# Performance work log

Hardware: AMD Instinct MI355X
Metric: run time of the kernel (lower is better)

## Reference

```python
import jax, jax.numpy as jnp
import numpy as np

KERNEL_SIZE = 5  # k, local correlation window
EPS = 1e-6


def local_self_correlation(x, k):
    """x: (b,c,h,w) -> (b,k^2,h,w). For each of the k^2 shifts (dy,dx) compute
    sum_c x[..., y+dy, x+dx] * x[..., y, x] with zero padding at borders."""
    pad = k // 2
    b, c, h, w = x.shape
    xp = jnp.pad(x, ((0, 0), (0, 0), (pad, pad), (pad, pad)))
    outs = []
    for dy in range(-pad, pad + 1):  # fixed small loop over k^2 shifts
        for dx in range(-pad, pad + 1):
            nb = xp[:, :, pad + dy:pad + dy + h, pad + dx:pad + dx + w]
            outs.append(jnp.sum(nb * x, axis=1))  # (b,h,w)
    return jnp.stack(outs, axis=1)  # (b,k^2,h,w)


def feature_l2norm(f):
    norm = jnp.sqrt(jnp.sum(f * f, axis=1, keepdims=True) + EPS)
    return f / norm


def setup_inputs() -> dict:
    key = jax.random.key(0)
    k1, k2, k3 = jax.random.split(key, 3)
    b, c, h, w = 8, 1024, 64, 64
    hidden = 1024
    in_dim = c + KERNEL_SIZE * KERNEL_SIZE  # 1049
    x = jax.random.normal(k1, (b, c, h, w), dtype=jnp.float32)
    W = jax.random.normal(k2, (hidden, in_dim), dtype=jnp.float32) * 0.02
    bias = jax.random.normal(k3, (hidden,), dtype=jnp.float32) * 0.02
    return {"x": x, "W": W, "b": bias}


def reference(x, W, b):
    feature_gs = local_self_correlation(x, KERNEL_SIZE)      # (b,k^2,h,w)
    feature_gs = feature_l2norm(feature_gs)
    feature_cat = jnp.concatenate([x, feature_gs], axis=1)    # (b,c+k^2,h,w)
    # 1x1 conv == channel GEMM, then ReLU
    out = jnp.einsum('bihw,oi->bohw', feature_cat, W) + b[None, :, None, None]
    return jax.nn.relu(out)
```

## Files before the change

### kernel.cpp

```cpp
#include <hip/hip_runtime.h>

typedef __attribute__((ext_vector_type(8))) short bf16x8;
typedef __attribute__((ext_vector_type(4))) float f32x4;

__device__ __forceinline__ unsigned short f2bf(float f) {
    unsigned int u = __float_as_uint(f);
    unsigned int r = (u + 0x7fffu + ((u >> 16) & 1u)) >> 16;
    return (unsigned short)r;
}

#define KPAD 1088
#define NT   17

__global__ void kWb_conv(const float* __restrict__ W, unsigned short* __restrict__ Wb)
{
    const int o = blockIdx.x;
    for (int k = threadIdx.x; k < KPAD; k += 256) {
        float v = (k < 1049) ? W[(size_t)o * 1049 + k] : 0.f;
        Wb[(size_t)o * KPAD + k] = f2bf(v);
    }
}

__global__ __launch_bounds__(256) void kT_conv(const float* __restrict__ x,
                                               unsigned short* __restrict__ xT)
{
    __shared__ unsigned short tile[64][128];
    const int bid = blockIdx.x;
    const int mst = bid >> 3;
    const int ct  = bid & 7;
    const int m0  = mst * 64;
    const int b   = m0 >> 12, ms0 = m0 & 4095;
    const int t   = threadIdx.x;
    const int msq = (t & 15) * 4;
    const int cg  = t >> 4;
    const int c0  = ct * 128 + cg * 8;

    const float* src = x + ((size_t)b * 1024 + c0) * 4096 + ms0 + msq;
    float4 v[8];
    #pragma unroll
    for (int j = 0; j < 8; ++j)
        v[j] = *(const float4*)(src + (size_t)j * 4096);

    #pragma unroll
    for (int p = 0; p < 4; ++p) {
        unsigned int w[4];
        #pragma unroll
        for (int q = 0; q < 4; ++q) {
            float lo = ((const float*)&v[2 * q])[p];
            float hi = ((const float*)&v[2 * q + 1])[p];
            w[q] = (unsigned int)f2bf(lo) | ((unsigned int)f2bf(hi) << 16);
        }
        const int row = msq + p;
        const int pch = cg ^ ((row >> 2) & 15);
        *(uint4*)&tile[row][pch * 8] = make_uint4(w[0], w[1], w[2], w[3]);
    }
    __syncthreads();

    #pragma unroll
    for (int q = 0; q < 4; ++q) {
        const int flat = q * 256 + t;
        const int row  = flat >> 4, ch = flat & 15;
        const int pch  = ch ^ ((row >> 2) & 15);
        uint4 val = *(const uint4*)&tile[row][pch * 8];
        *(uint4*)((char*)xT + (size_t)(m0 + row) * (KPAD * 2) + (size_t)(ct * 128 + ch * 8) * 2) = val;
    }
}

__global__ __launch_bounds__(256, 2) void k1a_corr(const float* __restrict__ x,
                                                   float* __restrict__ fpart)
{
    __shared__ float slab[2][20][68];
    const int bid   = blockIdx.x;
    const int split = bid & 15;
    const int b     = (bid >> 4) & 7;
    const int rg    = bid >> 7;
    const int y0    = rg * 16;
    const int t     = threadIdx.x;
    const int tc    = t & 15, tr = t >> 4;
    const int cs    = tc * 4;

    if (t < 160) {
        int buf = t / 80, rem = t % 80;
        int r = rem >> 2, cc = rem & 3;
        slab[buf][r][(cc < 2) ? cc : (64 + cc)] = 0.f;
    }

    float acc[25][4];
    #pragma unroll
    for (int s = 0; s < 25; ++s)
        #pragma unroll
        for (int p = 0; p < 4; ++p) acc[s][p] = 0.f;

    const float* xb = x + ((size_t)b * 1024 + split * 64) * 4096;

    const int r0 = t >> 4,         c40 = t & 15;
    const int y0r0 = y0 - 2 + r0;
    const int r1 = (t + 256) >> 4, c41 = t & 15;
    const int y0r1 = y0 - 2 + r1;
    const bool has1 = (t < 64);

    #define K1A_LOAD(ch, VA, VB)                                                \
        {                                                                        \
            const float* s_ = xb + (size_t)(ch) * 4096;                          \
            VA = (y0r0 >= 0 && y0r0 < 64) ? *(const float4*)(s_ + y0r0 * 64 + c40 * 4) \
                                          : make_float4(0.f, 0.f, 0.f, 0.f);     \
            if (has1)                                                            \
                VB = (y0r1 >= 0 && y0r1 < 64) ? *(const float4*)(s_ + y0r1 * 64 + c41 * 4) \
                                              : make_float4(0.f, 0.f, 0.f, 0.f); \
        }
    #define K1A_WRITE(buf, VA, VB)                                               \
        {                                                                        \
            float2* d0 = (float2*)&slab[buf][r0][2 + c40 * 4];                   \
            d0[0] = make_float2(VA.x, VA.y);                                     \
            d0[1] = make_float2(VA.z, VA.w);                                     \
            if (has1) {                                                          \
                float2* d1 = (float2*)&slab[buf][r1][2 + c41 * 4];               \
                d1[0] = make_float2(VB.x, VB.y);                                 \
                d1[1] = make_float2(VB.z, VB.w);                                 \
            }                                                                    \
        }
    #define K1A_COMPUTE(buf)                                                     \
        {                                                                        \
            const float* base = &slab[buf][tr][cs];                              \
            float ctr[4], wf[8];                                                 \
            {                                                                    \
                const float4* pr = (const float4*)(base + 2 * 68);               \
                float4 a = pr[0], b4 = pr[1];                                    \
                wf[0]=a.x; wf[1]=a.y; wf[2]=a.z; wf[3]=a.w;                      \
                wf[4]=b4.x; wf[5]=b4.y; wf[6]=b4.z; wf[7]=b4.w;                  \
                ctr[0]=wf[2]; ctr[1]=wf[3]; ctr[2]=wf[4]; ctr[3]=wf[5];          \
                _Pragma("unroll")                                                \
                for (int dx = -2; dx <= 2; ++dx)                                 \
                    _Pragma("unroll")                                            \
                    for (int p = 0; p < 4; ++p)                                  \
                        acc[10 + dx + 2][p] += wf[p + 2 + dx] * ctr[p];          \
            }                                                                    \
            _Pragma("unroll")                                                    \
            for (int r = 0; r < 5; ++r) {                                        \
                if (r == 2) continue;                                            \
                const float4* pr = (const float4*)(base + r * 68);               \
                float4 a = pr[0], b4 = pr[1];                                    \
                wf[0]=a.x; wf[1]=a.y; wf[2]=a.z; wf[3]=a.w;                      \
                wf[4]=b4.x; wf[5]=b4.y; wf[6]=b4.z; wf[7]=b4.w;                  \
                _Pragma("unroll")                                                \
                for (int dx = -2; dx <= 2; ++dx)                                 \
                    _Pragma("unroll")                                            \
                    for (int p = 0; p < 4; ++p)                                  \
                        acc[r * 5 + dx + 2][p] += wf[p + 2 + dx] * ctr[p];       \
            }                                                                    \
        }

    float4 Sa0, Sa1, Sb0, Sb1;
    K1A_LOAD(0, Sa0, Sa1)
    K1A_LOAD(1, Sb0, Sb1)
    K1A_WRITE(0, Sa0, Sa1)
    K1A_LOAD(2, Sa0, Sa1)
    __syncthreads();

    for (int i = 0; i < 64; i += 2) {
        K1A_WRITE(1, Sb0, Sb1)
        K1A_LOAD(min(i + 3, 63), Sb0, Sb1)
        K1A_COMPUTE(0)
        __syncthreads();
        K1A_WRITE(0, Sa0, Sa1)
        K1A_LOAD(min(i + 4, 63), Sa0, Sa1)
        K1A_COMPUTE(1)
        __syncthreads();
    }
    #undef K1A_LOAD
    #undef K1A_WRITE
    #undef K1A_COMPUTE

    const int mbase = b * 4096 + (y0 + tr) * 64 + cs;
    #pragma unroll
    for (int s = 0; s < 25; ++s) {
        *(float4*)(fpart + (size_t)(split * 25 + s) * 32768 + mbase) =
            make_float4(acc[s][0], acc[s][1], acc[s][2], acc[s][3]);
    }
}

__global__ void k1b_norm(const float* __restrict__ fpart, unsigned short* __restrict__ xT)
{
    const int m = blockIdx.x * 256 + threadIdx.x;
    float f[25];
    #pragma unroll
    for (int s = 0; s < 25; ++s) {
        float v = 0.f;
        #pragma unroll
        for (int sp = 0; sp < 16; ++sp)
            v += fpart[(size_t)(sp * 25 + s) * 32768 + m];
        f[s] = v;
    }
    float ss = 1e-6f;
    #pragma unroll
    for (int s = 0; s < 25; ++s) ss += f[s] * f[s];
    const float inv = 1.f / sqrtf(ss);

    unsigned int w[16];
    #pragma unroll
    for (int q = 0; q < 16; ++q) w[q] = 0u;
    #pragma unroll
    for (int s = 0; s < 25; ++s) {
        unsigned int h = f2bf(f[s] * inv);
        w[s >> 1] |= h << ((s & 1) * 16);
    }
    uint4* dst = (uint4*)((char*)xT + (size_t)m * (KPAD * 2) + 2048);
    dst[0] = make_uint4(w[0],  w[1],  w[2],  w[3]);
    dst[1] = make_uint4(w[4],  w[5],  w[6],  w[7]);
    dst[2] = make_uint4(w[8],  w[9],  w[10], w[11]);
    dst[3] = make_uint4(w[12], w[13], w[14], w[15]);
    uint4 z = make_uint4(0u, 0u, 0u, 0u);
    dst[4] = z; dst[5] = z; dst[6] = z; dst[7] = z;
}

__global__ __launch_bounds__(512, 2) void kgemm(const unsigned short* __restrict__ xT,
                                                const unsigned short* __restrict__ Wb,
                                                const float* __restrict__ bias,
                                                float* __restrict__ out)
{
    __shared__ unsigned short LA[2][256][64];
    __shared__ unsigned short LB[2][256][64];

    const int bid = blockIdx.x;
    const int wg  = (bid & 7) * 64 + (bid >> 3);
    const int mt  = wg >> 2, nt = wg & 3;
    const int m0  = mt * 256, n0 = nt * 256;
    const int t   = threadIdx.x;
    const int l   = t & 63, w = t >> 6;
    const int lr  = l & 15, kq = l >> 4;
    const int wm  = w >> 2, wn = w & 3;

    const int sr = l >> 3;
    const int sp = (l & 7) ^ sr;
    const unsigned short* gA = xT + (size_t)(m0 + w * 8 + sr) * KPAD + sp * 8;
    const unsigned short* gB = Wb + (size_t)(n0 + w * 8 + sr) * KPAD + sp * 8;

    auto STAGE = [&](int tt, int half) {
        if ((unsigned)tt >= NT) return;
        const int db = tt & 1;
        const size_t ko = (size_t)tt * 64;
        if (half < 2) {
            const unsigned short* g = gA + (size_t)(half * 128) * KPAD + ko;
            __builtin_amdgcn_global_load_lds((const void*)g,
                (void*)&LA[db][half * 128 + w * 8][0], 16, 0, 0);
            __builtin_amdgcn_global_load_lds((const void*)(g + (size_t)64 * KPAD),
                (void*)&LA[db][half * 128 + 64 + w * 8][0], 16, 0, 0);
        } else {
            const int hb = half - 2;
            const unsigned short* g = gB + (size_t)(hb * 128) * KPAD + ko;
            __builtin_amdgcn_global_load_lds((const void*)g,
                (void*)&LB[db][hb * 128 + w * 8][0], 16, 0, 0);
            __builtin_amdgcn_global_load_lds((const void*)(g + (size_t)64 * KPAD),
                (void*)&LB[db][hb * 128 + 64 + w * 8][0], 16, 0, 0);
        }
    };

    f32x4 zero = {0.f, 0.f, 0.f, 0.f};
    f32x4 acc[8][4];
    #pragma unroll
    for (int i = 0; i < 8; ++i)
        #pragma unroll
        for (int j = 0; j < 4; ++j) acc[i][j] = zero;

    bf16x8 a0[4][2], a1[4][2], b0[2][2], b1[2][2];

    #define LDA(dst, DB, ih)                                                     \
        _Pragma("unroll")                                                        \
        for (int i = 0; i < 4; ++i) {                                            \
            _Pragma("unroll")                                                    \
            for (int ks = 0; ks < 2; ++ks) {                                     \
                const int row = wm * 128 + ((ih) * 4 + i) * 16 + lr;             \
                const int slot = (ks * 4 + kq) ^ (row & 7);                      \
                dst[i][ks] = *(const bf16x8*)&LA[DB][row][slot * 8];             \
            }                                                                    \
        }
    #define LDB(dst, DB, jh)                                                     \
        _Pragma("unroll")                                                        \
        for (int j = 0; j < 2; ++j) {                                            \
            _Pragma("unroll")                                                    \
            for (int ks = 0; ks < 2; ++ks) {                                     \
                const int row = wn * 64 + ((jh) * 2 + j) * 16 + lr;              \
                const int slot = (ks * 4 + kq) ^ (row & 7);                      \
                dst[j][ks] = *(const bf16x8*)&LB[DB][row][slot * 8];             \
            }                                                                    \
        }
    #define MM(A, B, i0, j0)                                                     \
        _Pragma("unroll")                                                        \
        for (int ks = 0; ks < 2; ++ks) {                                         \
            _Pragma("unroll")                                                    \
            for (int i = 0; i < 4; ++i) {                                        \
                _Pragma("unroll")                                                \
                for (int j = 0; j < 2; ++j)                                      \
                    acc[(i0) + i][(j0) + j] = __builtin_amdgcn_mfma_f32_16x16x32_bf16( \
                        A[i][ks], B[j][ks], acc[(i0) + i][(j0) + j], 0, 0, 0);   \
            }                                                                    \
        }

    #define TILE(DB, TT)                                                         \
    {                                                                            \
        const int tti = (TT);                                                    \
                      \
        LDA(a0, DB, 0)                                                           \
        LDB(b0, DB, 0)                                                           \
        STAGE(tti + 1, 1);                                                       \
        asm volatile("s_waitcnt lgkmcnt(8)" ::: "memory");                       \
        __builtin_amdgcn_s_barrier();                                            \
        asm volatile("s_waitcnt lgkmcnt(0)" ::: "memory");                       \
        __builtin_amdgcn_sched_barrier(0);                                       \
        __builtin_amdgcn_s_setprio(1);                                           \
        MM(a0, b0, 0, 0)                                                         \
        __builtin_amdgcn_s_setprio(0);                                           \
        __builtin_amdgcn_s_barrier();                                            \
                      \
        LDA(a1, DB, 1)                                                           \
        LDB(b1, DB, 1)                                                           \
        STAGE(tti + 1, 3);                                                       \
        asm volatile("s_waitcnt lgkmcnt(8)" ::: "memory");                       \
        __builtin_amdgcn_s_barrier();                                            \
        asm volatile("s_waitcnt lgkmcnt(0)" ::: "memory");                       \
        __builtin_amdgcn_sched_barrier(0);                                       \
        __builtin_amdgcn_s_setprio(1);                                           \
        MM(a0, b1, 0, 2)                                                         \
        __builtin_amdgcn_s_setprio(0);                                           \
        __builtin_amdgcn_s_barrier();                                            \
            \
        STAGE(tti + 2, 0);                                                       \
        __builtin_amdgcn_s_barrier();                                            \
        __builtin_amdgcn_s_setprio(1);                                           \
        MM(a1, b0, 4, 0)                                                         \
        __builtin_amdgcn_s_setprio(0);                                           \
        __builtin_amdgcn_s_barrier();                                            \
             \
        STAGE(tti + 2, 2);                                                       \
        __builtin_amdgcn_s_barrier();                                            \
        __builtin_amdgcn_s_setprio(1);                                           \
        MM(a1, b1, 4, 2)                                                         \
        __builtin_amdgcn_s_setprio(0);                                           \
        if (tti + 2 < NT) {                                                      \
            asm volatile("s_waitcnt vmcnt(4)" ::: "memory");                     \
        } else {                                                                 \
            asm volatile("s_waitcnt vmcnt(0)" ::: "memory");                     \
        }                                                                        \
        __builtin_amdgcn_s_barrier();                                            \
    }

    STAGE(0, 0); STAGE(0, 2); STAGE(0, 1); STAGE(0, 3);
    STAGE(1, 0); STAGE(1, 2);
    asm volatile("s_waitcnt vmcnt(4)" ::: "memory");
    __builtin_amdgcn_s_barrier();

    int tt = 0;
    #pragma unroll 1
    for (int it = 0; it < (NT - 1) / 2; ++it, tt += 2) {
        TILE(0, tt)
        TILE(1, tt + 1)
    }
    TILE(0, NT - 1)

    const int bb = m0 >> 12;
    const int ms = (m0 & 4095) + wm * 128 + kq * 4;
    #pragma unroll
    for (int j = 0; j < 4; ++j) {
        const int n = n0 + wn * 64 + j * 16 + lr;
        const float bv = bias[n];
        float* ob = out + (size_t)bb * 4194304 + (size_t)n * 4096 + ms;
        #pragma unroll
        for (int i = 0; i < 8; ++i) {
            f32x4 v = acc[i][j];
            float4 o = make_float4(fmaxf(v[0] + bv, 0.f), fmaxf(v[1] + bv, 0.f),
                                   fmaxf(v[2] + bv, 0.f), fmaxf(v[3] + bv, 0.f));
            *(float4*)(ob + i * 16) = o;
        }
    }
    #undef LDA
    #undef LDB
    #undef MM
    #undef TILE
}

extern "C" void kernel_launch(void* const* d_in, const int* in_sizes, int n_in,
                              void* d_out, int out_size, void* d_ws, size_t ws_size,
                              hipStream_t stream)
{
    const float* x    = (const float*)d_in[0];
    const float* W    = (const float*)d_in[1];
    const float* bias = (const float*)d_in[2];
    float* out        = (float*)d_out;

    char* ws = (char*)d_ws;
    unsigned short* xT = (unsigned short*)ws;
    unsigned short* Wb = (unsigned short*)(ws + 71303168);
    float* fpart       = (float*)d_out;

    kWb_conv<<<1024, 256, 0, stream>>>(W, Wb);
    kT_conv <<<4096, 256, 0, stream>>>(x, xT);
    k1a_corr<<<512,  256, 0, stream>>>(x, fpart);
    k1b_norm<<<128,  256, 0, stream>>>(fpart, xT);
    kgemm   <<<512,  512, 0, stream>>>(xT, Wb, bias, out);
}
```

Before: 203.5 us.

## Merge front-end kernels into one launch and reorder GEMM tile MFMA phases

Merges the W bf16 conversion, the x transpose/convert, and the local correlation into a single kernel that branches on block index. The goal is to cut launch overhead and let the compute-heavy correlation blocks overlap with the memory-bound conversion blocks. Separately, the GEMM tile loop now runs its MFMA quadrants in a different order, and the A-fragment LDS load moves later, which shortens how long those registers stay live. The shared launch bounds of (256, 2) now apply to the conversion blocks too, and the combined kernel carries the correlation path's register pressure, which may lower occupancy for those blocks.

```diff
diff --git a/kernel.cpp b/kernel.cpp
--- a/kernel.cpp
+++ b/kernel.cpp
@@ -12,170 +12,170 @@
 #define KPAD 1088
 #define NT   17
 
-__global__ void kWb_conv(const float* __restrict__ W, unsigned short* __restrict__ Wb)
+__global__ __launch_bounds__(256, 2) void kfront(const float* __restrict__ x,
+                                                 const float* __restrict__ W,
+                                                 unsigned short* __restrict__ xT,
+                                                 unsigned short* __restrict__ Wb,
+                                                 float* __restrict__ fpart)
 {
-    const int o = blockIdx.x;
-    for (int k = threadIdx.x; k < KPAD; k += 256) {
-        float v = (k < 1049) ? W[(size_t)o * 1049 + k] : 0.f;
-        Wb[(size_t)o * KPAD + k] = f2bf(v);
-    }
-}
-
-__global__ __launch_bounds__(256) void kT_conv(const float* __restrict__ x,
-                                               unsigned short* __restrict__ xT)
-{
-    __shared__ unsigned short tile[64][128];
-    const int bid = blockIdx.x;
-    const int mst = bid >> 3;
-    const int ct  = bid & 7;
-    const int m0  = mst * 64;
-    const int b   = m0 >> 12, ms0 = m0 & 4095;
-    const int t   = threadIdx.x;
-    const int msq = (t & 15) * 4;
-    const int cg  = t >> 4;
-    const int c0  = ct * 128 + cg * 8;
-
-    const float* src = x + ((size_t)b * 1024 + c0) * 4096 + ms0 + msq;
-    float4 v[8];
-    #pragma unroll
-    for (int j = 0; j < 8; ++j)
-        v[j] = *(const float4*)(src + (size_t)j * 4096);
-
-    #pragma unroll
-    for (int p = 0; p < 4; ++p) {
-        unsigned int w[4];
+    __shared__ float4 lds_raw[1024];
+    const int gbid = blockIdx.x;
+    const int t    = threadIdx.x;
+
+    if (gbid < 512) {
+        float (*slab)[20][68] = (float (*)[20][68])lds_raw;
+        const int bid   = gbid;
+        const int split = bid & 15;
+        const int b     = (bid >> 4) & 7;
+        const int rg    = bid >> 7;
+        const int y0    = rg * 16;
+        const int tc    = t & 15, tr = t >> 4;
+        const int cs    = tc * 4;
+
+        if (t < 160) {
+            int buf = t / 80, rem = t % 80;
+            int r = rem >> 2, cc = rem & 3;
+            slab[buf][r][(cc < 2) ? cc : (64 + cc)] = 0.f;
+        }
+
+        float acc[25][4];
+        #pragma unroll
+        for (int s = 0; s < 25; ++s)
+            #pragma unroll
+            for (int p = 0; p < 4; ++p) acc[s][p] = 0.f;
+
+        const float* xb = x + ((size_t)b * 1024 + split * 64) * 4096;
+
+        const int r0 = t >> 4,         c40 = t & 15;
+        const int y0r0 = y0 - 2 + r0;
+        const int r1 = (t + 256) >> 4, c41 = t & 15;
+        const int y0r1 = y0 - 2 + r1;
+        const bool has1 = (t < 64);
+
+        #define K1A_LOAD(ch, VA, VB)                                                \
+            {                                                                        \
+                const float* s_ = xb + (size_t)(ch) * 4096;                          \
+                VA = (y0r0 >= 0 && y0r0 < 64) ? *(const float4*)(s_ + y0r0 * 64 + c40 * 4) \
+                                              : make_float4(0.f, 0.f, 0.f, 0.f);     \
+                if (has1)                                                            \
+                    VB = (y0r1 >= 0 && y0r1 < 64) ? *(const float4*)(s_ + y0r1 * 64 + c41 * 4) \
+                                                  : make_float4(0.f, 0.f, 0.f, 0.f); \
+            }
+        #define K1A_WRITE(buf, VA, VB)                                               \
+            {                                                                        \
+                float2* d0 = (float2*)&slab[buf][r0][2 + c40 * 4];                   \
+                d0[0] = make_float2(VA.x, VA.y);                                     \
+                d0[1] = make_float2(VA.z, VA.w);                                     \
+                if (has1) {                                                          \
+                    float2* d1 = (float2*)&slab[buf][r1][2 + c41 * 4];               \
+                    d1[0] = make_float2(VB.x, VB.y);                                 \
+                    d1[1] = make_float2(VB.z, VB.w);                                 \
+                }                                                                    \
+            }
+        #define K1A_COMPUTE(buf)                                                     \
+            {                                                                        \
+                const float* base = &slab[buf][tr][cs];                              \
+                float ctr[4], wf[8];                                                 \
+                {                                                                    \
+                    const float4* pr = (const float4*)(base + 2 * 68);               \
+                    float4 a = pr[0], b4 = pr[1];                                    \
+                    wf[0]=a.x; wf[1]=a.y; wf[2]=a.z; wf[3]=a.w;                      \
+                    wf[4]=b4.x; wf[5]=b4.y; wf[6]=b4.z; wf[7]=b4.w;                  \
+                    ctr[0]=wf[2]; ctr[1]=wf[3]; ctr[2]=wf[4]; ctr[3]=wf[5];          \
+                    _Pragma("unroll")                                                \
+                    for (int dx = -2; dx <= 2; ++dx)                                 \
+                        _Pragma("unroll")                                            \
+                        for (int p = 0; p < 4; ++p)                                  \
+                            acc[10 + dx + 2][p] += wf[p + 2 + dx] * ctr[p];          \
+                }                                                                    \
+                _Pragma("unroll")                                                    \
+                for (int r = 0; r < 5; ++r) {                                        \
+                    if (r == 2) continue;                                            \
+                    const float4* pr = (const float4*)(base + r * 68);               \
+                    float4 a = pr[0], b4 = pr[1];                                    \
+                    wf[0]=a.x; wf[1]=a.y; wf[2]=a.z; wf[3]=a.w;                      \
+                    wf[4]=b4.x; wf[5]=b4.y; wf[6]=b4.z; wf[7]=b4.w;                  \
+                    _Pragma("unroll")                                                \
+                    for (int dx = -2; dx <= 2; ++dx)                                 \
+                        _Pragma("unroll")                                            \
+                        for (int p = 0; p < 4; ++p)                                  \
+                            acc[r * 5 + dx + 2][p] += wf[p + 2 + dx] * ctr[p];       \
+                }                                                                    \
+            }
+
+        float4 Sa0, Sa1, Sb0, Sb1;
+        K1A_LOAD(0, Sa0, Sa1)
+        K1A_LOAD(1, Sb0, Sb1)
+        K1A_WRITE(0, Sa0, Sa1)
+        K1A_LOAD(2, Sa0, Sa1)
+        __syncthreads();
+
+        for (int i = 0; i < 64; i += 2) {
+            K1A_WRITE(1, Sb0, Sb1)
+            K1A_LOAD(min(i + 3, 63), Sb0, Sb1)
+            K1A_COMPUTE(0)
+            __syncthreads();
+            K1A_WRITE(0, Sa0, Sa1)
+            K1A_LOAD(min(i + 4, 63), Sa0, Sa1)
+            K1A_COMPUTE(1)
+            __syncthreads();
+        }
+        #undef K1A_LOAD
+        #undef K1A_WRITE
+        #undef K1A_COMPUTE
+
+        const int mbase = b * 4096 + (y0 + tr) * 64 + cs;
+        #pragma unroll
+        for (int s = 0; s < 25; ++s) {
+            *(float4*)(fpart + (size_t)(split * 25 + s) * 32768 + mbase) =
+                make_float4(acc[s][0], acc[s][1], acc[s][2], acc[s][3]);
+        }
+    } else if (gbid < 4608) {
+        unsigned short (*tile)[128] = (unsigned short (*)[128])lds_raw;
+        const int bid = gbid - 512;
+        const int mst = bid >> 3;
+        const int ct  = bid & 7;
+        const int m0  = mst * 64;
+        const int b   = m0 >> 12, ms0 = m0 & 4095;
+        const int msq = (t & 15) * 4;
+        const int cg  = t >> 4;
+        const int c0  = ct * 128 + cg * 8;
+
+        const float* src = x + ((size_t)b * 1024 + c0) * 4096 + ms0 + msq;
+        float4 v[8];
+        #pragma unroll
+        for (int j = 0; j < 8; ++j)
+            v[j] = *(const float4*)(src + (size_t)j * 4096);
+
+        #pragma unroll
+        for (int p = 0; p < 4; ++p) {
+            unsigned int w[4];
+            #pragma unroll
+            for (int q = 0; q < 4; ++q) {
+                float lo = ((const float*)&v[2 * q])[p];
+                float hi = ((const float*)&v[2 * q + 1])[p];
+                w[q] = (unsigned int)f2bf(lo) | ((unsigned int)f2bf(hi) << 16);
+            }
+            const int row = msq + p;
+            const int pch = cg ^ ((row >> 2) & 15);
+            *(uint4*)&tile[row][pch * 8] = make_uint4(w[0], w[1], w[2], w[3]);
+        }
+        __syncthreads();
+
         #pragma unroll
         for (int q = 0; q < 4; ++q) {
-            float lo = ((const float*)&v[2 * q])[p];
-            float hi = ((const float*)&v[2 * q + 1])[p];
-            w[q] = (unsigned int)f2bf(lo) | ((unsigned int)f2bf(hi) << 16);
-        }
-        const int row = msq + p;
-        const int pch = cg ^ ((row >> 2) & 15);
-        *(uint4*)&tile[row][pch * 8] = make_uint4(w[0], w[1], w[2], w[3]);
-    }
-    __syncthreads();
-
-    #pragma unroll
-    for (int q = 0; q < 4; ++q) {
-        const int flat = q * 256 + t;
-        const int row  = flat >> 4, ch = flat & 15;
-        const int pch  = ch ^ ((row >> 2) & 15);
-        uint4 val = *(const uint4*)&tile[row][pch * 8];
-        *(uint4*)((char*)xT + (size_t)(m0 + row) * (KPAD * 2) + (size_t)(ct * 128 + ch * 8) * 2) = val;
-    }
-}
-
-__global__ __launch_bounds__(256, 2) void k1a_corr(const float* __restrict__ x,
-                                                   float* __restrict__ fpart)
-{
-    __shared__ float slab[2][20][68];
-    const int bid   = blockIdx.x;
-    const int split = bid & 15;
-    const int b     = (bid >> 4) & 7;
-    const int rg    = bid >> 7;
-    const int y0    = rg * 16;
-    const int t     = threadIdx.x;
-    const int tc    = t & 15, tr = t >> 4;
-    const int cs    = tc * 4;
-
-    if (t < 160) {
-        int buf = t / 80, rem = t % 80;
-        int r = rem >> 2, cc = rem & 3;
-        slab[buf][r][(cc < 2) ? cc : (64 + cc)] = 0.f;
-    }
-
-    float acc[25][4];
-    #pragma unroll
-    for (int s = 0; s < 25; ++s)
-        #pragma unroll
-        for (int p = 0; p < 4; ++p) acc[s][p] = 0.f;
-
-    const float* xb = x + ((size_t)b * 1024 + split * 64) * 4096;
-
-    const int r0 = t >> 4,         c40 = t & 15;
-    const int y0r0 = y0 - 2 + r0;
-    const int r1 = (t + 256) >> 4, c41 = t & 15;
-    const int y0r1 = y0 - 2 + r1;
-    const bool has1 = (t < 64);
-
-    #define K1A_LOAD(ch, VA, VB)                                                \
-        {                                                                        \
-            const float* s_ = xb + (size_t)(ch) * 4096;                          \
-            VA = (y0r0 >= 0 && y0r0 < 64) ? *(const float4*)(s_ + y0r0 * 64 + c40 * 4) \
-                                          : make_float4(0.f, 0.f, 0.f, 0.f);     \
-            if (has1)                                                            \
-                VB = (y0r1 >= 0 && y0r1 < 64) ? *(const float4*)(s_ + y0r1 * 64 + c41 * 4) \
-                                              : make_float4(0.f, 0.f, 0.f, 0.f); \
-        }
-    #define K1A_WRITE(buf, VA, VB)                                               \
-        {                                                                        \
-            float2* d0 = (float2*)&slab[buf][r0][2 + c40 * 4];                   \
-            d0[0] = make_float2(VA.x, VA.y);                                     \
-            d0[1] = make_float2(VA.z, VA.w);                                     \
-            if (has1) {                                                          \
-                float2* d1 = (float2*)&slab[buf][r1][2 + c41 * 4];               \
-                d1[0] = make_float2(VB.x, VB.y);                                 \
-                d1[1] = make_float2(VB.z, VB.w);                                 \
-            }                                                                    \
-        }
-    #define K1A_COMPUTE(buf)                                                     \
-        {                                                                        \
-            const float* base = &slab[buf][tr][cs];                              \
-            float ctr[4], wf[8];                                                 \
-            {                                                                    \
-                const float4* pr = (const float4*)(base + 2 * 68);               \
-                float4 a = pr[0], b4 = pr[1];                                    \
-                wf[0]=a.x; wf[1]=a.y; wf[2]=a.z; wf[3]=a.w;                      \
-                wf[4]=b4.x; wf[5]=b4.y; wf[6]=b4.z; wf[7]=b4.w;                  \
-                ctr[0]=wf[2]; ctr[1]=wf[3]; ctr[2]=wf[4]; ctr[3]=wf[5];          \
-                _Pragma("unroll")                                                \
-                for (int dx = -2; dx <= 2; ++dx)                                 \
-                    _Pragma("unroll")                                            \
-                    for (int p = 0; p < 4; ++p)                                  \
-                        acc[10 + dx + 2][p] += wf[p + 2 + dx] * ctr[p];          \
-            }                                                                    \
-            _Pragma("unroll")                                                    \
-            for (int r = 0; r < 5; ++r) {                                        \
-                if (r == 2) continue;                                            \
-                const float4* pr = (const float4*)(base + r * 68);               \
-                float4 a = pr[0], b4 = pr[1];                                    \
-                wf[0]=a.x; wf[1]=a.y; wf[2]=a.z; wf[3]=a.w;                      \
-                wf[4]=b4.x; wf[5]=b4.y; wf[6]=b4.z; wf[7]=b4.w;                  \
-                _Pragma("unroll")                                                \
-                for (int dx = -2; dx <= 2; ++dx)                                 \
-                    _Pragma("unroll")                                            \
-                    for (int p = 0; p < 4; ++p)                                  \
-                        acc[r * 5 + dx + 2][p] += wf[p + 2 + dx] * ctr[p];       \
-            }                                                                    \
-        }
-
-    float4 Sa0, Sa1, Sb0, Sb1;
-    K1A_LOAD(0, Sa0, Sa1)
-    K1A_LOAD(1, Sb0, Sb1)
-    K1A_WRITE(0, Sa0, Sa1)
-    K1A_LOAD(2, Sa0, Sa1)
-    __syncthreads();
-
-    for (int i = 0; i < 64; i += 2) {
-        K1A_WRITE(1, Sb0, Sb1)
-        K1A_LOAD(min(i + 3, 63), Sb0, Sb1)
-        K1A_COMPUTE(0)
-        __syncthreads();
-        K1A_WRITE(0, Sa0, Sa1)
-        K1A_LOAD(min(i + 4, 63), Sa0, Sa1)
-        K1A_COMPUTE(1)
-        __syncthreads();
-    }
-    #undef K1A_LOAD
-    #undef K1A_WRITE
-    #undef K1A_COMPUTE
-
-    const int mbase = b * 4096 + (y0 + tr) * 64 + cs;
-    #pragma unroll
-    for (int s = 0; s < 25; ++s) {
-        *(float4*)(fpart + (size_t)(split * 25 + s) * 32768 + mbase) =
-            make_float4(acc[s][0], acc[s][1], acc[s][2], acc[s][3]);
+            const int flat = q * 256 + t;
+            const int row  = flat >> 4, ch = flat & 15;
+            const int pch  = ch ^ ((row >> 2) & 15);
+            uint4 val = *(const uint4*)&tile[row][pch * 8];
+            *(uint4*)((char*)xT + (size_t)(m0 + row) * (KPAD * 2) + (size_t)(ct * 128 + ch * 8) * 2) = val;
+        }
+    } else {
+        const int o = gbid - 4608;
+        for (int k = t; k < KPAD; k += 256) {
+            float v = (k < 1049) ? W[(size_t)o * 1049 + k] : 0.f;
+            Wb[(size_t)o * KPAD + k] = f2bf(v);
+        }
     }
 }
 
@@ -299,7 +299,7 @@
     #define TILE(DB, TT)                                                         \
     {                                                                            \
         const int tti = (TT);                                                    \
-                      \
+                          \
         LDA(a0, DB, 0)                                                           \
         LDB(b0, DB, 0)                                                           \
         STAGE(tti + 1, 1);                                                       \
@@ -311,11 +311,9 @@
         MM(a0, b0, 0, 0)                                                         \
         __builtin_amdgcn_s_setprio(0);                                           \
         __builtin_amdgcn_s_barrier();                                            \
-                      \
-        LDA(a1, DB, 1)                                                           \
+                                \
         LDB(b1, DB, 1)                                                           \
         STAGE(tti + 1, 3);                                                       \
-        asm volatile("s_waitcnt lgkmcnt(8)" ::: "memory");                       \
         __builtin_amdgcn_s_barrier();                                            \
         asm volatile("s_waitcnt lgkmcnt(0)" ::: "memory");                       \
         __builtin_amdgcn_sched_barrier(0);                                       \
@@ -323,18 +321,21 @@
         MM(a0, b1, 0, 2)                                                         \
         __builtin_amdgcn_s_setprio(0);                                           \
         __builtin_amdgcn_s_barrier();                                            \
+           \
+        LDA(a1, DB, 1)                                                           \
+        STAGE(tti + 2, 0);                                                       \
+        __builtin_amdgcn_s_barrier();                                            \
+        asm volatile("s_waitcnt lgkmcnt(0)" ::: "memory");                       \
+        __builtin_amdgcn_sched_barrier(0);                                       \
+        __builtin_amdgcn_s_setprio(1);                                           \
+        MM(a1, b1, 4, 2)                                                         \
+        __builtin_amdgcn_s_setprio(0);                                           \
+        __builtin_amdgcn_s_barrier();                                            \
             \
-        STAGE(tti + 2, 0);                                                       \
+        STAGE(tti + 2, 2);                                                       \
         __builtin_amdgcn_s_barrier();                                            \
         __builtin_amdgcn_s_setprio(1);                                           \
         MM(a1, b0, 4, 0)                                                         \
-        __builtin_amdgcn_s_setprio(0);                                           \
-        __builtin_amdgcn_s_barrier();                                            \
-             \
-        STAGE(tti + 2, 2);                                                       \
-        __builtin_amdgcn_s_barrier();                                            \
-        __builtin_amdgcn_s_setprio(1);                                           \
-        MM(a1, b1, 4, 2)                                                         \
         __builtin_amdgcn_s_setprio(0);                                           \
         if (tti + 2 < NT) {                                                      \
             asm volatile("s_waitcnt vmcnt(4)" ::: "memory");                     \
@@ -392,9 +393,7 @@
     unsigned short* Wb = (unsigned short*)(ws + 71303168);
     float* fpart       = (float*)d_out;
 
-    kWb_conv<<<1024, 256, 0, stream>>>(W, Wb);
-    kT_conv <<<4096, 256, 0, stream>>>(x, xT);
-    k1a_corr<<<512,  256, 0, stream>>>(x, fpart);
+    kfront <<<5632, 256, 0, stream>>>(x, W, xT, Wb, fpart);
     k1b_norm<<<128,  256, 0, stream>>>(fpart, xT);
-    kgemm   <<<512,  512, 0, stream>>>(xT, Wb, bias, out);
-}
+    kgemm  <<<512,  512, 0, stream>>>(xT, Wb, bias, out);
+}
```

Result: faster. 192.4 us (-5.5%).

## Deepen correlation prefetch to 4 stages and reorder GEMM fragment loads

Applied to the files above, without the earlier changes.

The correlation kernel now keeps four register stages of global loads in flight instead of two. It also replaces the full __syncthreads with an LDS-wait plus raw barrier, one per step, so global load latency is hidden further ahead. In the GEMM tile, the A1 fragment load is deferred until after the first two MFMA blocks. The MFMA quadrant order changes to a0b0, a0b1, a1b1, a1b0, which spreads LDS reads across phases and reduces register pressure from holding both A fragments at once. The deeper prefetch uses more registers, which may hurt occupancy.

```diff
diff --git a/kernel.cpp b/kernel.cpp
--- a/kernel.cpp
+++ b/kernel.cpp
@@ -149,27 +149,36 @@
                         acc[r * 5 + dx + 2][p] += wf[p + 2 + dx] * ctr[p];       \
             }                                                                    \
         }
-
-    float4 Sa0, Sa1, Sb0, Sb1;
-    K1A_LOAD(0, Sa0, Sa1)
-    K1A_LOAD(1, Sb0, Sb1)
-    K1A_WRITE(0, Sa0, Sa1)
-    K1A_LOAD(2, Sa0, Sa1)
-    __syncthreads();
-
-    for (int i = 0; i < 64; i += 2) {
-        K1A_WRITE(1, Sb0, Sb1)
-        K1A_LOAD(min(i + 3, 63), Sb0, Sb1)
-        K1A_COMPUTE(0)
-        __syncthreads();
-        K1A_WRITE(0, Sa0, Sa1)
-        K1A_LOAD(min(i + 4, 63), Sa0, Sa1)
-        K1A_COMPUTE(1)
-        __syncthreads();
+    #define K1A_BAR()                                                            \
+        asm volatile("s_waitcnt lgkmcnt(0)" ::: "memory");                       \
+        __builtin_amdgcn_s_barrier();
+
+    #define K1A_BODY(i, RN0, RN1, RC0, RC1)                                      \
+        if ((i) + 1 < 64) { K1A_WRITE(((i) + 1) & 1, RN0, RN1) }                 \
+        K1A_LOAD(min((i) + 4, 63), RC0, RC1)                                     \
+        K1A_COMPUTE((i) & 1)                                                     \
+        K1A_BAR()
+
+    float4 A0, A1, B0, B1, C0, C1, D0, D1;
+    K1A_LOAD(0, A0, A1)
+    K1A_LOAD(1, B0, B1)
+    K1A_LOAD(2, C0, C1)
+    K1A_LOAD(3, D0, D1)
+    K1A_WRITE(0, A0, A1)
+    K1A_BAR()
+
+    #pragma unroll 1
+    for (int ii = 0; ii < 64; ii += 4) {
+        K1A_BODY(ii + 0, B0, B1, A0, A1)
+        K1A_BODY(ii + 1, C0, C1, B0, B1)
+        K1A_BODY(ii + 2, D0, D1, C0, C1)
+        K1A_BODY(ii + 3, A0, A1, D0, D1)
     }
     #undef K1A_LOAD
     #undef K1A_WRITE
     #undef K1A_COMPUTE
+    #undef K1A_BAR
+    #undef K1A_BODY
 
     const int mbase = b * 4096 + (y0 + tr) * 64 + cs;
     #pragma unroll
@@ -299,7 +308,7 @@
     #define TILE(DB, TT)                                                         \
     {                                                                            \
         const int tti = (TT);                                                    \
-                      \
+                          \
         LDA(a0, DB, 0)                                                           \
         LDB(b0, DB, 0)                                                           \
         STAGE(tti + 1, 1);                                                       \
@@ -311,11 +320,9 @@
         MM(a0, b0, 0, 0)                                                         \
         __builtin_amdgcn_s_setprio(0);                                           \
         __builtin_amdgcn_s_barrier();                                            \
-                      \
-        LDA(a1, DB, 1)                                                           \
+                                \
         LDB(b1, DB, 1)                                                           \
         STAGE(tti + 1, 3);                                                       \
-        asm volatile("s_waitcnt lgkmcnt(8)" ::: "memory");                       \
         __builtin_amdgcn_s_barrier();                                            \
         asm volatile("s_waitcnt lgkmcnt(0)" ::: "memory");                       \
         __builtin_amdgcn_sched_barrier(0);                                       \
@@ -323,18 +330,21 @@
         MM(a0, b1, 0, 2)                                                         \
         __builtin_amdgcn_s_setprio(0);                                           \
         __builtin_amdgcn_s_barrier();                                            \
+           \
+        LDA(a1, DB, 1)                                                           \
+        STAGE(tti + 2, 0);                                                       \
+        __builtin_amdgcn_s_barrier();                                            \
+        asm volatile("s_waitcnt lgkmcnt(0)" ::: "memory");                       \
+        __builtin_amdgcn_sched_barrier(0);                                       \
+        __builtin_amdgcn_s_setprio(1);                                           \
+        MM(a1, b1, 4, 2)                                                         \
+        __builtin_amdgcn_s_setprio(0);                                           \
+        __builtin_amdgcn_s_barrier();                                            \
             \
-        STAGE(tti + 2, 0);                                                       \
+        STAGE(tti + 2, 2);                                                       \
         __builtin_amdgcn_s_barrier();                                            \
         __builtin_amdgcn_s_setprio(1);                                           \
         MM(a1, b0, 4, 0)                                                         \
-        __builtin_amdgcn_s_setprio(0);                                           \
-        __builtin_amdgcn_s_barrier();                                            \
-             \
-        STAGE(tti + 2, 2);                                                       \
-        __builtin_amdgcn_s_barrier();                                            \
-        __builtin_amdgcn_s_setprio(1);                                           \
-        MM(a1, b1, 4, 2)                                                         \
         __builtin_amdgcn_s_setprio(0);                                           \
         if (tti + 2 < NT) {                                                      \
             asm volatile("s_waitcnt vmcnt(4)" ::: "memory");                     \
```

Result: slower. 260.9 us (+28.2%).
